# Kernel tuning notes

Measured on AMD Instinct MI355X. Metric: run time of the kernel, lower is better.

The kernel has to match this reference:

```python
import jax, jax.numpy as jnp
import numpy as np

B, Q, C = 2, 300, 80       # batch, queries, classes
MH, MW = 128, 128          # model mask resolution
OUT_H, OUT_W = 512, 512    # target image size (consistent across batch)


def setup_inputs() -> dict:
    key = jax.random.key(0)
    k1, k2, k3, k4 = jax.random.split(key, 4)
    return {
        "pred_logits": jax.random.normal(k1, (B, Q, C), jnp.float32),
        "pred_boxes": jax.random.uniform(k2, (B, Q, 4), jnp.float32),  # cxcywh in [0,1]
        "pred_masks": jax.random.normal(k3, (B, Q, MH, MW), jnp.float32),
        "presence_logit_dec": jax.random.normal(k4, (B, C), jnp.float32),
        "target_sizes_boxes": jnp.full((B, 2), 512, jnp.int32),
        "target_sizes_masks": jnp.full((B, 2), OUT_H, jnp.int32),
    }


def _box_cxcywh_to_xyxy(b):
    cx, cy, w, h = jnp.split(b, 4, axis=-1)
    return jnp.concatenate([cx - 0.5 * w, cy - 0.5 * h, cx + 0.5 * w, cy + 0.5 * h], axis=-1)


def reference(pred_logits, pred_boxes, pred_masks, presence_logit_dec,
              target_sizes_boxes, target_sizes_masks):
    # scores: sigmoid(class logits) * sigmoid(presence logit) broadcast over queries
    probs = jax.nn.sigmoid(pred_logits) * jax.nn.sigmoid(presence_logit_dec)[:, None, :]  # [B,Q,C]
    scores = probs.max(-1)                                   # [B,Q]
    labels = jnp.ones(scores.shape, jnp.int32)               # forced_labels is None -> ones_like

    # boxes: cxcywh -> xyxy, scaled per-image by [w, h, w, h]
    boxes = _box_cxcywh_to_xyxy(pred_boxes)                  # [B,Q,4]
    img_h = target_sizes_boxes[:, 0].astype(boxes.dtype)
    img_w = target_sizes_boxes[:, 1].astype(boxes.dtype)
    scale_fct = jnp.stack([img_w, img_h, img_w, img_h], axis=1)  # [B,4]
    boxes = boxes * scale_fct[:, None, :]

    # masks: bilinear upsample (align_corners=False == half-pixel centers),
    # then sigmoid + 0.5 threshold -> bool. consistent=True branch (static out size).
    masks = jax.image.resize(
        pred_masks,
        (pred_masks.shape[0], pred_masks.shape[1], OUT_H, OUT_W),
        method="bilinear",
    )
    masks = jax.nn.sigmoid(masks) > 0.5                      # [B,Q,OUT_H,OUT_W] bool

    return scores, labels, boxes, masks
```

## Files before the change

kernel.cpp:

```cpp
#include <hip/hip_runtime.h>
#include <math.h>

#define NB 2
#define NQ 300
#define NC 80
#define MH 128
#define MW 128
#define OUT_H 512
#define OUT_W 512

#define OFF_SCORES 0
#define OFF_LABELS (NB*NQ)
#define OFF_BOXES  (2*NB*NQ)
#define OFF_MASKS  (6*NB*NQ)

__device__ __forceinline__ float sigf(float x) {
    return 1.0f / (1.0f + expf(-x));
}

__global__ __launch_bounds__(256)
void sbl_kernel(const float* __restrict__ logits,
                const float* __restrict__ boxes,
                const float* __restrict__ presence,
                const int*   __restrict__ ts_boxes,
                float* __restrict__ out) {
    int i = blockIdx.x * blockDim.x + threadIdx.x;
    if (i >= NB * NQ) return;
    int b = i / NQ;

    const float* lg = logits + (size_t)i * NC;
    const float* pr = presence + (size_t)b * NC;
    float best = -1e30f;
    #pragma unroll 8
    for (int c = 0; c < NC; ++c) {
        float s = sigf(lg[c]) * sigf(pr[c]);
        best = fmaxf(best, s);
    }
    out[OFF_SCORES + i] = best;
    out[OFF_LABELS + i] = 1.0f;

    const float* bx = boxes + (size_t)i * 4;
    float cx = bx[0], cy = bx[1], w = bx[2], h = bx[3];
    float img_h = (float)ts_boxes[b * 2 + 0];
    float img_w = (float)ts_boxes[b * 2 + 1];
    float* ob = out + OFF_BOXES + (size_t)i * 4;
    ob[0] = (cx - 0.5f * w) * img_w;
    ob[1] = (cy - 0.5f * h) * img_h;
    ob[2] = (cx + 0.5f * w) * img_w;
    ob[3] = (cy + 0.5f * h) * img_h;
}

__global__ __launch_bounds__(256)
void mask_kernel(const float* __restrict__ pm, float* __restrict__ out) {
    int lid = threadIdx.x;
    int r = blockIdx.x * 2 + (lid >> 7);
    int t = lid & 127;
    int bq = r >> 9;
    int y  = r & 511;

    float sy = 0.25f * (float)y - 0.375f;
    int y0 = (int)floorf(sy);
    double fy = (double)sy - (double)y0;
    int y0c = max(y0, 0);
    int y1c = min(y0 + 1, MH - 1);

    const float* base = pm + (size_t)bq * (MH * MW);
    const float* r0 = base + (size_t)y0c * MW;
    const float* r1 = base + (size_t)y1c * MW;

    int c0 = max(t - 1, 0);
    int c2 = min(t + 1, MW - 1);

    double w1 = fy, w0 = 1.0 - fy;
    double a = (double)r0[c0] * w0 + (double)r1[c0] * w1;
    double b = (double)r0[t]  * w0 + (double)r1[t]  * w1;
    double c = (double)r0[c2] * w0 + (double)r1[c2] * w1;

    float4 o;
    o.x = (a * 0.375 + b * 0.625) > 0.0 ? 1.0f : 0.0f;
    o.y = (a * 0.125 + b * 0.875) > 0.0 ? 1.0f : 0.0f;
    o.z = (b * 0.875 + c * 0.125) > 0.0 ? 1.0f : 0.0f;
    o.w = (b * 0.625 + c * 0.375) > 0.0 ? 1.0f : 0.0f;

    float4* outp = (float4*)(out + OFF_MASKS + (size_t)r * OUT_W + (size_t)t * 4);
    *outp = o;
}

extern "C" void kernel_launch(void* const* d_in, const int* in_sizes, int n_in,
                              void* d_out, int out_size, void* d_ws, size_t ws_size,
                              hipStream_t stream) {
    const float* pred_logits   = (const float*)d_in[0];
    const float* pred_boxes    = (const float*)d_in[1];
    const float* pred_masks    = (const float*)d_in[2];
    const float* presence      = (const float*)d_in[3];
    const int*   ts_boxes      = (const int*)d_in[4];
    (void)d_in[5]; (void)in_sizes; (void)n_in; (void)out_size; (void)d_ws; (void)ws_size;

    float* out = (float*)d_out;

    sbl_kernel<<<(NB * NQ + 255) / 256, 256, 0, stream>>>(
        pred_logits, pred_boxes, presence, ts_boxes, out);

    int rows = NB * NQ * OUT_H;
    mask_kernel<<<rows / 2, 256, 0, stream>>>(pred_masks, out);
}
```

Before: 690.5 us.

## Compute four output rows per thread, use fp32 math and nontemporal stores

Each thread now owns one input row position and emits the four output rows that derive from it, loading a 3x3 neighborhood once instead of re-reading two input rows per output row. The double-precision blend is replaced with fp32 arithmetic, and outputs go out through nontemporal vector stores to avoid polluting cache with the large write-only mask. The work is dominated by writing the mask, so the gain depends mostly on store efficiency. fp32 rounding could flip threshold decisions for values very near zero.

Result: faster. 664.7 us (-3.7%).

```diff
diff --git a/kernel.cpp b/kernel.cpp
--- a/kernel.cpp
+++ b/kernel.cpp
@@ -13,6 +13,8 @@
 #define OFF_LABELS (NB*NQ)
 #define OFF_BOXES  (2*NB*NQ)
 #define OFF_MASKS  (6*NB*NQ)
+
+typedef float f32x4 __attribute__((ext_vector_type(4)));
 
 __device__ __forceinline__ float sigf(float x) {
     return 1.0f / (1.0f + expf(-x));
@@ -53,37 +55,43 @@
 __global__ __launch_bounds__(256)
 void mask_kernel(const float* __restrict__ pm, float* __restrict__ out) {
     int lid = threadIdx.x;
-    int r = blockIdx.x * 2 + (lid >> 7);
+    int pidx = blockIdx.x * 2 + (lid >> 7);
     int t = lid & 127;
-    int bq = r >> 9;
-    int y  = r & 511;
-
-    float sy = 0.25f * (float)y - 0.375f;
-    int y0 = (int)floorf(sy);
-    double fy = (double)sy - (double)y0;
-    int y0c = max(y0, 0);
-    int y1c = min(y0 + 1, MH - 1);
+    int bq = pidx >> 7;
+    int m  = pidx & 127;
 
     const float* base = pm + (size_t)bq * (MH * MW);
-    const float* r0 = base + (size_t)y0c * MW;
-    const float* r1 = base + (size_t)y1c * MW;
+    int rA = (m == 0)      ? 0       : m - 1;
+    int rC = (m == MH - 1) ? MH - 1  : m + 1;
+    const float* rowA = base + (size_t)rA * MW;
+    const float* rowB = base + (size_t)m  * MW;
+    const float* rowC = base + (size_t)rC * MW;
 
-    int c0 = max(t - 1, 0);
-    int c2 = min(t + 1, MW - 1);
+    int c0 = (t == 0)      ? 0      : t - 1;
+    int c2 = (t == MW - 1) ? MW - 1 : t + 1;
 
-    double w1 = fy, w0 = 1.0 - fy;
-    double a = (double)r0[c0] * w0 + (double)r1[c0] * w1;
-    double b = (double)r0[t]  * w0 + (double)r1[t]  * w1;
-    double c = (double)r0[c2] * w0 + (double)r1[c2] * w1;
+    float A0 = rowA[c0], A1 = rowA[t], A2 = rowA[c2];
+    float B0 = rowB[c0], B1 = rowB[t], B2 = rowB[c2];
+    float C0 = rowC[c0], C1 = rowC[t], C2 = rowC[c2];
 
-    float4 o;
-    o.x = (a * 0.375 + b * 0.625) > 0.0 ? 1.0f : 0.0f;
-    o.y = (a * 0.125 + b * 0.875) > 0.0 ? 1.0f : 0.0f;
-    o.z = (b * 0.875 + c * 0.125) > 0.0 ? 1.0f : 0.0f;
-    o.w = (b * 0.625 + c * 0.375) > 0.0 ? 1.0f : 0.0f;
+    float* dst = out + OFF_MASKS + (((size_t)bq * OUT_H + 4 * m) * OUT_W + 4 * t);
 
-    float4* outp = (float4*)(out + OFF_MASKS + (size_t)r * OUT_W + (size_t)t * 4);
-    *outp = o;
+    #pragma unroll
+    for (int j = 0; j < 4; ++j) {
+        float p, q, r;
+        if (j == 0)      { p = A0*0.375f + B0*0.625f; q = A1*0.375f + B1*0.625f; r = A2*0.375f + B2*0.625f; }
+        else if (j == 1) { p = A0*0.125f + B0*0.875f; q = A1*0.125f + B1*0.875f; r = A2*0.125f + B2*0.875f; }
+        else if (j == 2) { p = B0*0.875f + C0*0.125f; q = B1*0.875f + C1*0.125f; r = B2*0.875f + C2*0.125f; }
+        else             { p = B0*0.625f + C0*0.375f; q = B1*0.625f + C1*0.375f; r = B2*0.625f + C2*0.375f; }
+
+        f32x4 o;
+        o.x = (p*0.375f + q*0.625f) > 0.0f ? 1.0f : 0.0f;
+        o.y = (p*0.125f + q*0.875f) > 0.0f ? 1.0f : 0.0f;
+        o.z = (q*0.875f + r*0.125f) > 0.0f ? 1.0f : 0.0f;
+        o.w = (q*0.625f + r*0.375f) > 0.0f ? 1.0f : 0.0f;
+
+        __builtin_nontemporal_store(o, (f32x4*)(dst + (size_t)j * OUT_W));
+    }
 }
 
 extern "C" void kernel_launch(void* const* d_in, const int* in_sizes, int n_in,
@@ -94,13 +102,12 @@
     const float* pred_masks    = (const float*)d_in[2];
     const float* presence      = (const float*)d_in[3];
     const int*   ts_boxes      = (const int*)d_in[4];
-    (void)d_in[5]; (void)in_sizes; (void)n_in; (void)out_size; (void)d_ws; (void)ws_size;
+    (void)in_sizes; (void)n_in; (void)out_size; (void)d_ws; (void)ws_size;
 
     float* out = (float*)d_out;
 
     sbl_kernel<<<(NB * NQ + 255) / 256, 256, 0, stream>>>(
         pred_logits, pred_boxes, presence, ts_boxes, out);
 
-    int rows = NB * NQ * OUT_H;
-    mask_kernel<<<rows / 2, 256, 0, stream>>>(pred_masks, out);
+    mask_kernel<<<NB * NQ * MH / 2, 256, 0, stream>>>(pred_masks, out);
 }
```

## Split mask upsampling into bit-packed compute pass and streaming float expansion pass

Applied to the files above, without the earlier changes.

Mask generation now runs in two stages. The first computes the bilinear threshold in fp32 instead of fp64 and packs 32 output pixels into one bit word in workspace. The second is a grid-stride kernel that expands the bits into float4 outputs using nontemporal stores. The goal is to separate compute from the large 629 MB output write stream and drop the fp64 math, at the cost of an extra launch and a small workspace round trip. The fp32 math may flip pixels whose interpolated value is very close to zero.

Result: slower. 706.6 us (+2.3%).

```diff
diff --git a/kernel.cpp b/kernel.cpp
--- a/kernel.cpp
+++ b/kernel.cpp
@@ -13,6 +13,14 @@
 #define OFF_LABELS (NB*NQ)
 #define OFF_BOXES  (2*NB*NQ)
 #define OFF_MASKS  (6*NB*NQ)
+
+#define WORDS_PER_ROW 16
+#define WORDS_PER_IMG (OUT_H * WORDS_PER_ROW)
+
+#define EXP_BLOCKS 3840
+#define EXP_ITERS  40
+
+typedef float f32x4 __attribute__((ext_vector_type(4)));
 
 __device__ __forceinline__ float sigf(float x) {
     return 1.0f / (1.0f + expf(-x));
@@ -51,39 +59,63 @@
 }
 
 __global__ __launch_bounds__(256)
-void mask_kernel(const float* __restrict__ pm, float* __restrict__ out) {
-    int lid = threadIdx.x;
-    int r = blockIdx.x * 2 + (lid >> 7);
-    int t = lid & 127;
-    int bq = r >> 9;
-    int y  = r & 511;
+void mask_bits_kernel(const float* __restrict__ pm, unsigned int* __restrict__ bits_out) {
+    int tid = blockIdx.x * 256 + threadIdx.x;
+    int w  = tid & 15;
+    int y  = (tid >> 4) & 511;
+    int bq = tid >> 13;
 
     float sy = 0.25f * (float)y - 0.375f;
     int y0 = (int)floorf(sy);
-    double fy = (double)sy - (double)y0;
-    int y0c = max(y0, 0);
-    int y1c = min(y0 + 1, MH - 1);
+    float fy = sy - (float)y0;
+    int r0 = max(y0, 0);
+    int r1 = min(y0 + 1, MH - 1);
 
     const float* base = pm + (size_t)bq * (MH * MW);
-    const float* r0 = base + (size_t)y0c * MW;
-    const float* r1 = base + (size_t)y1c * MW;
+    const float* rowA = base + (size_t)r0 * MW;
+    const float* rowB = base + (size_t)r1 * MW;
 
-    int c0 = max(t - 1, 0);
-    int c2 = min(t + 1, MW - 1);
+    float w1 = fy, w0 = 1.0f - fy;
+    float c[10];
+    int cbase = 8 * w - 1;
+    #pragma unroll
+    for (int k = 0; k < 10; ++k) {
+        int col = cbase + k;
+        col = col < 0 ? 0 : (col > MW - 1 ? MW - 1 : col);
+        c[k] = rowA[col] * w0 + rowB[col] * w1;
+    }
 
-    double w1 = fy, w0 = 1.0 - fy;
-    double a = (double)r0[c0] * w0 + (double)r1[c0] * w1;
-    double b = (double)r0[t]  * w0 + (double)r1[t]  * w1;
-    double c = (double)r0[c2] * w0 + (double)r1[c2] * w1;
+    unsigned int bits = 0;
+    #pragma unroll
+    for (int g = 0; g < 8; ++g) {
+        float p = c[g], q = c[g + 1], r = c[g + 2];
+        unsigned int b0 = (p * 0.375f + q * 0.625f) > 0.0f ? 1u : 0u;
+        unsigned int b1 = (p * 0.125f + q * 0.875f) > 0.0f ? 1u : 0u;
+        unsigned int b2 = (q * 0.875f + r * 0.125f) > 0.0f ? 1u : 0u;
+        unsigned int b3 = (q * 0.625f + r * 0.375f) > 0.0f ? 1u : 0u;
+        bits |= (b0 | (b1 << 1) | (b2 << 2) | (b3 << 3)) << (4 * g);
+    }
+    bits_out[tid] = bits;
+}
 
-    float4 o;
-    o.x = (a * 0.375 + b * 0.625) > 0.0 ? 1.0f : 0.0f;
-    o.y = (a * 0.125 + b * 0.875) > 0.0 ? 1.0f : 0.0f;
-    o.z = (b * 0.875 + c * 0.125) > 0.0 ? 1.0f : 0.0f;
-    o.w = (b * 0.625 + c * 0.375) > 0.0 ? 1.0f : 0.0f;
+__global__ __launch_bounds__(256)
+void mask_expand_kernel(const unsigned int* __restrict__ bits_in, float* __restrict__ out) {
+    const int gstride = EXP_BLOCKS * 256;
+    int gtid = blockIdx.x * 256 + threadIdx.x;
+    float* mout = out + OFF_MASKS;
 
-    float4* outp = (float4*)(out + OFF_MASKS + (size_t)r * OUT_W + (size_t)t * 4);
-    *outp = o;
+    #pragma unroll 4
+    for (int it = 0; it < EXP_ITERS; ++it) {
+        int idx = gtid + it * gstride;
+        unsigned int word = bits_in[idx >> 3];
+        unsigned int n = (word >> ((idx & 7) * 4)) & 0xFu;
+        f32x4 o;
+        o.x = (n & 1u) ? 1.0f : 0.0f;
+        o.y = (n & 2u) ? 1.0f : 0.0f;
+        o.z = (n & 4u) ? 1.0f : 0.0f;
+        o.w = (n & 8u) ? 1.0f : 0.0f;
+        __builtin_nontemporal_store(o, (f32x4*)(mout + (size_t)idx * 4));
+    }
 }
 
 extern "C" void kernel_launch(void* const* d_in, const int* in_sizes, int n_in,
@@ -94,13 +126,16 @@
     const float* pred_masks    = (const float*)d_in[2];
     const float* presence      = (const float*)d_in[3];
     const int*   ts_boxes      = (const int*)d_in[4];
-    (void)d_in[5]; (void)in_sizes; (void)n_in; (void)out_size; (void)d_ws; (void)ws_size;
+    (void)in_sizes; (void)n_in; (void)out_size; (void)ws_size;
 
     float* out = (float*)d_out;
+    unsigned int* bits = (unsigned int*)d_ws;
 
     sbl_kernel<<<(NB * NQ + 255) / 256, 256, 0, stream>>>(
         pred_logits, pred_boxes, presence, ts_boxes, out);
 
-    int rows = NB * NQ * OUT_H;
-    mask_kernel<<<rows / 2, 256, 0, stream>>>(pred_masks, out);
+    mask_bits_kernel<<<NB * NQ * OUT_H * WORDS_PER_ROW / 256, 256, 0, stream>>>(
+        pred_masks, bits);
+
+    mask_expand_kernel<<<EXP_BLOCKS, 256, 0, stream>>>(bits, out);
 }
```
